# Kernel optimization log

Measured on AMD Instinct MI355X. Metric: run time of the kernel, lower is better.

The kernel has to match this reference:

```python
import jax, jax.numpy as jnp
import numpy as np

EPS = 1e-6  # nn.PairwiseDistance default eps, added as x - y + eps before the norm


def setup_inputs() -> dict:
    key = jax.random.key(0)
    k1, k2 = jax.random.split(key)
    class_prototypes = jax.random.normal(k1, (1024, 1024), dtype=jnp.float32)
    query_features = jax.random.normal(k2, (8192, 1024), dtype=jnp.float32)
    return {"class_prototypes": class_prototypes, "query_features": query_features}


def reference(class_prototypes, query_features):
    # dist[i,k] = || q_i - p_k + EPS ||_2  (PairwiseDistance semantics)
    # expand: ||q||^2 + ||p||^2 - 2 q.p + 2*EPS*(sum q - sum p) + D*EPS^2
    D = query_features.shape[1]
    q_sq = jnp.sum(query_features * query_features, axis=1)        # [Q]
    p_sq = jnp.sum(class_prototypes * class_prototypes, axis=1)    # [K]
    cross = query_features @ class_prototypes.T                    # [Q,K]
    lin = 2.0 * EPS * (jnp.sum(query_features, axis=1)[:, None]
                       - jnp.sum(class_prototypes, axis=1)[None, :])
    sq = q_sq[:, None] + p_sq[None, :] - 2.0 * cross + lin + D * EPS * EPS
    dist = jnp.sqrt(jnp.maximum(sq, 0.0))                          # [Q,K]
    post = jnp.exp(-dist)
    post = post / jnp.sum(post, axis=1, keepdims=True)
    c = jnp.max(post, axis=1)
    h = -jnp.sum(post * jnp.log(post), axis=1)
    return (post, c, h)
```

## Files before the change

### kernel.cpp

```cpp
#include <hip/hip_runtime.h>
#include <hip/hip_bf16.h>

#define EPS 1e-6f

typedef float  f32x4  __attribute__((ext_vector_type(4)));
typedef __bf16 bf16x8 __attribute__((ext_vector_type(8)));

static __device__ __forceinline__ unsigned short f2bf(float f) {
    unsigned int x = __float_as_uint(f);
    unsigned int r = (x + 0x7FFFu + ((x >> 16) & 1u)) >> 16;
    return (unsigned short)r;
}
static __device__ __forceinline__ float bf2f(unsigned short u) {
    return __uint_as_float((unsigned int)u << 16);
}

__global__ __launch_bounds__(256) void prep_kernel(
    const float* __restrict__ protos, const float* __restrict__ querys,
    unsigned short* __restrict__ pb, unsigned short* __restrict__ qb,
    float* __restrict__ p_sq, float* __restrict__ p_sum,
    float* __restrict__ q_sq, float* __restrict__ q_sum)
{
    const int b   = blockIdx.x;
    const int tid = threadIdx.x;
    const float* src; unsigned short* dst; float* rsq; float* rsum;
    if (b < 1024) {
        src = protos + (size_t)b * 1024; dst = pb + (size_t)b * 1024;
        rsq = p_sq + b; rsum = p_sum + b;
    } else {
        const int r = b - 1024;
        src = querys + (size_t)r * 1024; dst = qb + (size_t)r * 1024;
        rsq = q_sq + r; rsum = q_sum + r;
    }

    const float4 v = reinterpret_cast<const float4*>(src)[tid];
    float s  = v.x + v.y + v.z + v.w;
    float ss = v.x * v.x + v.y * v.y + v.z * v.z + v.w * v.w;

    ushort4 o;
    o.x = f2bf(v.x); o.y = f2bf(v.y); o.z = f2bf(v.z); o.w = f2bf(v.w);
    reinterpret_cast<ushort4*>(dst)[tid] = o;

    #pragma unroll
    for (int m = 32; m >= 1; m >>= 1) {
        s  += __shfl_xor(s, m, 64);
        ss += __shfl_xor(ss, m, 64);
    }
    __shared__ float red[8];
    const int wave = tid >> 6;
    if ((tid & 63) == 0) { red[wave] = s; red[4 + wave] = ss; }
    __syncthreads();
    if (tid == 0) {
        *rsum = red[0] + red[1] + red[2] + red[3];
        *rsq  = red[4] + red[5] + red[6] + red[7];
    }
}

__global__ __launch_bounds__(256, 2) void gemm_exp_kernel(
    const unsigned short* __restrict__ qb,
    const unsigned short* __restrict__ pb,
    const float* __restrict__ q_sq, const float* __restrict__ q_sum,
    const float* __restrict__ p_sq, const float* __restrict__ p_sum,
    unsigned short* __restrict__ e_out,
    float* __restrict__ row_s, float* __restrict__ row_t,
    unsigned int* __restrict__ row_m)
{
    __shared__ unsigned short As[128 * 32];
    __shared__ unsigned short Bs[128 * 32];

    const int tid  = threadIdx.x;
    const int lane = tid & 63;
    const int wave = tid >> 6;
    const int wr = wave >> 1, wc = wave & 1;
    const int l15 = lane & 15;
    const int l4  = lane >> 4;
    const int br = blockIdx.x, bc = blockIdx.y;

    f32x4 acc[4][4];
    #pragma unroll
    for (int m = 0; m < 4; ++m)
        #pragma unroll
        for (int n = 0; n < 4; ++n)
            acc[m][n] = (f32x4)0.0f;

    const size_t qbase = (size_t)(br * 128) * 1024;
    const size_t pbase = (size_t)(bc * 128) * 1024;
    const int c0 = tid, c1 = tid + 256;

    for (int kk = 0; kk < 1024; kk += 32) {
        __syncthreads();
        {
            const unsigned short* gq0 = qb + qbase + (size_t)(c0 >> 2) * 1024 + kk + (c0 & 3) * 8;
            const unsigned short* gq1 = qb + qbase + (size_t)(c1 >> 2) * 1024 + kk + (c1 & 3) * 8;
            const unsigned short* gp0 = pb + pbase + (size_t)(c0 >> 2) * 1024 + kk + (c0 & 3) * 8;
            const unsigned short* gp1 = pb + pbase + (size_t)(c1 >> 2) * 1024 + kk + (c1 & 3) * 8;
            __builtin_amdgcn_global_load_lds((const __attribute__((address_space(1))) void*)gq0,
                                             (__attribute__((address_space(3))) void*)(&As[c0 * 8]), 16, 0, 0);
            __builtin_amdgcn_global_load_lds((const __attribute__((address_space(1))) void*)gq1,
                                             (__attribute__((address_space(3))) void*)(&As[c1 * 8]), 16, 0, 0);
            __builtin_amdgcn_global_load_lds((const __attribute__((address_space(1))) void*)gp0,
                                             (__attribute__((address_space(3))) void*)(&Bs[c0 * 8]), 16, 0, 0);
            __builtin_amdgcn_global_load_lds((const __attribute__((address_space(1))) void*)gp1,
                                             (__attribute__((address_space(3))) void*)(&Bs[c1 * 8]), 16, 0, 0);
        }
        __syncthreads();

        bf16x8 a[4], b[4];
        #pragma unroll
        for (int m = 0; m < 4; ++m)
            a[m] = *reinterpret_cast<const bf16x8*>(&As[(wr * 64 + m * 16 + l15) * 32 + l4 * 8]);
        #pragma unroll
        for (int n = 0; n < 4; ++n)
            b[n] = *reinterpret_cast<const bf16x8*>(&Bs[(wc * 64 + n * 16 + l15) * 32 + l4 * 8]);
        #pragma unroll
        for (int m = 0; m < 4; ++m)
            #pragma unroll
            for (int n = 0; n < 4; ++n)
                acc[m][n] = __builtin_amdgcn_mfma_f32_16x16x32_bf16(a[m], b[n], acc[m][n], 0, 0, 0);
    }

    const int row0 = br * 128 + wr * 64;
    const int col0 = bc * 128 + wc * 64;

    float ps[4], pm[4];
    #pragma unroll
    for (int n = 0; n < 4; ++n) {
        const int c = col0 + n * 16 + l15;
        ps[n] = p_sq[c];
        pm[n] = p_sum[c];
    }
    const float dee = 1024.0f * EPS * EPS;

    #pragma unroll
    for (int m = 0; m < 4; ++m) {
        #pragma unroll
        for (int r = 0; r < 4; ++r) {
            const int row = row0 + m * 16 + l4 * 4 + r;
            const float qs = q_sq[row], qm = q_sum[row];
            float se = 0.0f, te = 0.0f, mx = 0.0f;
            #pragma unroll
            for (int n = 0; n < 4; ++n) {
                const float cross = acc[m][n][r];
                const float sq = qs + ps[n] - 2.0f * cross + 2.0f * EPS * (qm - pm[n]) + dee;
                const float dist = sqrtf(fmaxf(sq, 0.0f));
                const float e = __expf(-dist);
                e_out[(size_t)row * 1024 + (col0 + n * 16 + l15)] = f2bf(e);
                se += e;
                te += e * dist;
                mx = fmaxf(mx, e);
            }
            #pragma unroll
            for (int msk = 8; msk >= 1; msk >>= 1) {
                se += __shfl_xor(se, msk, 64);
                te += __shfl_xor(te, msk, 64);
                mx = fmaxf(mx, __shfl_xor(mx, msk, 64));
            }
            if (l15 == 0) {
                atomicAdd(&row_s[row], se);
                atomicAdd(&row_t[row], te);
                atomicMax(&row_m[row], __float_as_uint(mx));
            }
        }
    }
}

__global__ __launch_bounds__(256) void normfin_kernel(
    const unsigned short* __restrict__ e16,
    const float* __restrict__ row_s, const float* __restrict__ row_t,
    const unsigned int* __restrict__ row_m,
    float* __restrict__ post, float* __restrict__ c_out, float* __restrict__ h_out)
{
    const int row = blockIdx.x;
    const int tid = threadIdx.x;
    const float s   = row_s[row];
    const float inv = 1.0f / s;
    if (tid == 0) {
        c_out[row] = __uint_as_float(row_m[row]) * inv;
        h_out[row] = logf(s) + row_t[row] * inv;
    }
    const ushort4 ev = reinterpret_cast<const ushort4*>(e16 + (size_t)row * 1024)[tid];
    float4 o;
    o.x = bf2f(ev.x) * inv;
    o.y = bf2f(ev.y) * inv;
    o.z = bf2f(ev.z) * inv;
    o.w = bf2f(ev.w) * inv;
    reinterpret_cast<float4*>(post + (size_t)row * 1024)[tid] = o;
}

extern "C" void kernel_launch(void* const* d_in, const int* in_sizes, int n_in,
                              void* d_out, int out_size, void* d_ws, size_t ws_size,
                              hipStream_t stream) {
    const float* protos = (const float*)d_in[0];
    const float* querys = (const float*)d_in[1];

    float* out   = (float*)d_out;
    float* post  = out;
    float* c_out = out + (size_t)8192 * 1024;
    float* h_out = c_out + 8192;

    char* ws = (char*)d_ws;
    unsigned short* qb  = (unsigned short*)ws;  ws += (size_t)8192 * 1024 * 2;
    unsigned short* pb  = (unsigned short*)ws;  ws += (size_t)1024 * 1024 * 2;
    unsigned short* e16 = (unsigned short*)ws;  ws += (size_t)8192 * 1024 * 2;
    float* q_sq  = (float*)ws;  ws += 8192 * 4;
    float* q_sum = (float*)ws;  ws += 8192 * 4;
    float* p_sq  = (float*)ws;  ws += 1024 * 4;
    float* p_sum = (float*)ws;  ws += 1024 * 4;
    float* row_s = (float*)ws;  ws += 8192 * 4;
    float* row_t = (float*)ws;  ws += 8192 * 4;
    unsigned int* row_m = (unsigned int*)ws;  ws += 8192 * 4;

    (void)hipMemsetAsync(row_s, 0, 3 * 8192 * sizeof(float), stream);

    prep_kernel<<<9216, 256, 0, stream>>>(protos, querys, pb, qb, p_sq, p_sum, q_sq, q_sum);
    gemm_exp_kernel<<<dim3(64, 8), 256, 0, stream>>>(qb, pb, q_sq, q_sum, p_sq, p_sum,
                                                     e16, row_s, row_t, row_m);
    normfin_kernel<<<8192, 256, 0, stream>>>(e16, row_s, row_t, row_m, post, c_out, h_out);
}
```

Before: 132.4 us.

## Fuse GEMM-exp and normalization into one cooperative kernel with grid sync

Merges the GEMM/exp kernel and the normalization kernel into a single cooperative launch. The exp values stay in accumulator registers across a grid-wide sync and are then scaled by the reciprocal row sum and written directly as fp32 post. This removes the bf16 intermediate round trip through global memory and one kernel launch. In exchange it adds a grid barrier and requires all 512 blocks to be co-resident. It also changes precision slightly, since post is no longer quantized through bf16.

Result: slower. 201.2 us (+52.0%).

```diff
diff --git a/kernel.cpp b/kernel.cpp
--- a/kernel.cpp
+++ b/kernel.cpp
@@ -1,5 +1,8 @@
 #include <hip/hip_runtime.h>
 #include <hip/hip_bf16.h>
+#include <hip/hip_cooperative_groups.h>
+
+namespace cg = cooperative_groups;
 
 #define EPS 1e-6f
 
@@ -10,9 +13,6 @@
     unsigned int x = __float_as_uint(f);
     unsigned int r = (x + 0x7FFFu + ((x >> 16) & 1u)) >> 16;
     return (unsigned short)r;
-}
-static __device__ __forceinline__ float bf2f(unsigned short u) {
-    return __uint_as_float((unsigned int)u << 16);
 }
 
 __global__ __launch_bounds__(256) void prep_kernel(
@@ -56,14 +56,14 @@
     }
 }
 
-__global__ __launch_bounds__(256, 2) void gemm_exp_kernel(
+__global__ __launch_bounds__(256, 2) void coop_kernel(
     const unsigned short* __restrict__ qb,
     const unsigned short* __restrict__ pb,
     const float* __restrict__ q_sq, const float* __restrict__ q_sum,
     const float* __restrict__ p_sq, const float* __restrict__ p_sum,
-    unsigned short* __restrict__ e_out,
     float* __restrict__ row_s, float* __restrict__ row_t,
-    unsigned int* __restrict__ row_m)
+    unsigned int* __restrict__ row_m,
+    float* __restrict__ post, float* __restrict__ c_out, float* __restrict__ h_out)
 {
     __shared__ unsigned short As[128 * 32];
     __shared__ unsigned short Bs[128 * 32];
@@ -144,7 +144,7 @@
                 const float sq = qs + ps[n] - 2.0f * cross + 2.0f * EPS * (qm - pm[n]) + dee;
                 const float dist = sqrtf(fmaxf(sq, 0.0f));
                 const float e = __expf(-dist);
-                e_out[(size_t)row * 1024 + (col0 + n * 16 + l15)] = f2bf(e);
+                acc[m][n][r] = e;
                 se += e;
                 te += e * dist;
                 mx = fmaxf(mx, e);
@@ -162,29 +162,29 @@
             }
         }
     }
-}
-
-__global__ __launch_bounds__(256) void normfin_kernel(
-    const unsigned short* __restrict__ e16,
-    const float* __restrict__ row_s, const float* __restrict__ row_t,
-    const unsigned int* __restrict__ row_m,
-    float* __restrict__ post, float* __restrict__ c_out, float* __restrict__ h_out)
-{
-    const int row = blockIdx.x;
-    const int tid = threadIdx.x;
-    const float s   = row_s[row];
-    const float inv = 1.0f / s;
-    if (tid == 0) {
+
+    cg::this_grid().sync();
+
+    #pragma unroll
+    for (int m = 0; m < 4; ++m) {
+        #pragma unroll
+        for (int r = 0; r < 4; ++r) {
+            const int row = row0 + m * 16 + l4 * 4 + r;
+            const float inv = 1.0f / row_s[row];
+            #pragma unroll
+            for (int n = 0; n < 4; ++n) {
+                post[(size_t)row * 1024 + (col0 + n * 16 + l15)] = acc[m][n][r] * inv;
+            }
+        }
+    }
+
+    if (bc == 0 && tid < 128) {
+        const int row = br * 128 + tid;
+        const float s   = row_s[row];
+        const float inv = 1.0f / s;
         c_out[row] = __uint_as_float(row_m[row]) * inv;
         h_out[row] = logf(s) + row_t[row] * inv;
     }
-    const ushort4 ev = reinterpret_cast<const ushort4*>(e16 + (size_t)row * 1024)[tid];
-    float4 o;
-    o.x = bf2f(ev.x) * inv;
-    o.y = bf2f(ev.y) * inv;
-    o.z = bf2f(ev.z) * inv;
-    o.w = bf2f(ev.w) * inv;
-    reinterpret_cast<float4*>(post + (size_t)row * 1024)[tid] = o;
 }
 
 extern "C" void kernel_launch(void* const* d_in, const int* in_sizes, int n_in,
@@ -199,9 +199,8 @@
     float* h_out = c_out + 8192;
 
     char* ws = (char*)d_ws;
-    unsigned short* qb  = (unsigned short*)ws;  ws += (size_t)8192 * 1024 * 2;
-    unsigned short* pb  = (unsigned short*)ws;  ws += (size_t)1024 * 1024 * 2;
-    unsigned short* e16 = (unsigned short*)ws;  ws += (size_t)8192 * 1024 * 2;
+    unsigned short* qb = (unsigned short*)ws;  ws += (size_t)8192 * 1024 * 2;
+    unsigned short* pb = (unsigned short*)ws;  ws += (size_t)1024 * 1024 * 2;
     float* q_sq  = (float*)ws;  ws += 8192 * 4;
     float* q_sum = (float*)ws;  ws += 8192 * 4;
     float* p_sq  = (float*)ws;  ws += 1024 * 4;
@@ -213,7 +212,10 @@
     (void)hipMemsetAsync(row_s, 0, 3 * 8192 * sizeof(float), stream);
 
     prep_kernel<<<9216, 256, 0, stream>>>(protos, querys, pb, qb, p_sq, p_sum, q_sq, q_sum);
-    gemm_exp_kernel<<<dim3(64, 8), 256, 0, stream>>>(qb, pb, q_sq, q_sum, p_sq, p_sum,
-                                                     e16, row_s, row_t, row_m);
-    normfin_kernel<<<8192, 256, 0, stream>>>(e16, row_s, row_t, row_m, post, c_out, h_out);
-}
+
+    void* args[] = { (void*)&qb, (void*)&pb, (void*)&q_sq, (void*)&q_sum,
+                     (void*)&p_sq, (void*)&p_sum, (void*)&row_s, (void*)&row_t,
+                     (void*)&row_m, (void*)&post, (void*)&c_out, (void*)&h_out };
+    (void)hipLaunchCooperativeKernel((const void*)coop_kernel, dim3(64, 8), dim3(256),
+                                     args, 0, stream);
+}
```

## Shrink GEMM tile to 128x64, swizzle LDS, and remap blocks for L2 locality

Applied to the files above, without the earlier changes.

Halves the prototype tile width so the GEMM launches 1024 blocks instead of 512, and raises the occupancy hint to 4 blocks per CU. It also XOR-swizzles the K-chunk placement in LDS to reduce bank conflicts on fragment reads. Block ids are remapped so that blocks scheduled together share query rows. The smaller tile lowers arithmetic intensity per LDS load, and the tighter launch bound may cause register pressure.

Measured after the change: 136.8 us. +3.3%, slower.

```diff
diff --git a/kernel.cpp b/kernel.cpp
--- a/kernel.cpp
+++ b/kernel.cpp
@@ -56,7 +56,7 @@
     }
 }
 
-__global__ __launch_bounds__(256, 2) void gemm_exp_kernel(
+__global__ __launch_bounds__(256, 4) void gemm_exp_kernel(
     const unsigned short* __restrict__ qb,
     const unsigned short* __restrict__ pb,
     const float* __restrict__ q_sq, const float* __restrict__ q_sum,
@@ -66,7 +66,7 @@
     unsigned int* __restrict__ row_m)
 {
     __shared__ unsigned short As[128 * 32];
-    __shared__ unsigned short Bs[128 * 32];
+    __shared__ unsigned short Bs[64 * 32];
 
     const int tid  = threadIdx.x;
     const int lane = tid & 63;
@@ -74,57 +74,65 @@
     const int wr = wave >> 1, wc = wave & 1;
     const int l15 = lane & 15;
     const int l4  = lane >> 4;
-    const int br = blockIdx.x, bc = blockIdx.y;
-
-    f32x4 acc[4][4];
+
+    const int hwid  = blockIdx.x + blockIdx.y * 64;
+    const int newid = (hwid & 7) * 128 + (hwid >> 3);
+    const int bx = newid >> 4;
+    const int by = newid & 15;
+
+    f32x4 acc[4][2];
     #pragma unroll
     for (int m = 0; m < 4; ++m)
         #pragma unroll
-        for (int n = 0; n < 4; ++n)
+        for (int n = 0; n < 2; ++n)
             acc[m][n] = (f32x4)0.0f;
 
-    const size_t qbase = (size_t)(br * 128) * 1024;
-    const size_t pbase = (size_t)(bc * 128) * 1024;
-    const int c0 = tid, c1 = tid + 256;
+    const size_t qbase = (size_t)(bx * 128) * 1024;
+    const size_t pbase = (size_t)(by * 64) * 1024;
 
     for (int kk = 0; kk < 1024; kk += 32) {
         __syncthreads();
         {
-            const unsigned short* gq0 = qb + qbase + (size_t)(c0 >> 2) * 1024 + kk + (c0 & 3) * 8;
-            const unsigned short* gq1 = qb + qbase + (size_t)(c1 >> 2) * 1024 + kk + (c1 & 3) * 8;
-            const unsigned short* gp0 = pb + pbase + (size_t)(c0 >> 2) * 1024 + kk + (c0 & 3) * 8;
-            const unsigned short* gp1 = pb + pbase + (size_t)(c1 >> 2) * 1024 + kk + (c1 & 3) * 8;
-            __builtin_amdgcn_global_load_lds((const __attribute__((address_space(1))) void*)gq0,
-                                             (__attribute__((address_space(3))) void*)(&As[c0 * 8]), 16, 0, 0);
-            __builtin_amdgcn_global_load_lds((const __attribute__((address_space(1))) void*)gq1,
-                                             (__attribute__((address_space(3))) void*)(&As[c1 * 8]), 16, 0, 0);
-            __builtin_amdgcn_global_load_lds((const __attribute__((address_space(1))) void*)gp0,
-                                             (__attribute__((address_space(3))) void*)(&Bs[c0 * 8]), 16, 0, 0);
-            __builtin_amdgcn_global_load_lds((const __attribute__((address_space(1))) void*)gp1,
-                                             (__attribute__((address_space(3))) void*)(&Bs[c1 * 8]), 16, 0, 0);
+            const int la0 = tid,      la1 = tid + 256, lb = tid;
+            const int kpa0 = (la0 & 3) ^ ((la0 >> 3) & 3);
+            const int kpa1 = (la1 & 3) ^ ((la1 >> 3) & 3);
+            const int kpb  = (lb  & 3) ^ ((lb  >> 3) & 3);
+            const unsigned short* ga0 = qb + qbase + (size_t)(la0 >> 2) * 1024 + kk + kpa0 * 8;
+            const unsigned short* ga1 = qb + qbase + (size_t)(la1 >> 2) * 1024 + kk + kpa1 * 8;
+            const unsigned short* gb  = pb + pbase + (size_t)(lb  >> 2) * 1024 + kk + kpb  * 8;
+            __builtin_amdgcn_global_load_lds((const __attribute__((address_space(1))) void*)ga0,
+                                             (__attribute__((address_space(3))) void*)(&As[la0 * 8]), 16, 0, 0);
+            __builtin_amdgcn_global_load_lds((const __attribute__((address_space(1))) void*)ga1,
+                                             (__attribute__((address_space(3))) void*)(&As[la1 * 8]), 16, 0, 0);
+            __builtin_amdgcn_global_load_lds((const __attribute__((address_space(1))) void*)gb,
+                                             (__attribute__((address_space(3))) void*)(&Bs[lb * 8]), 16, 0, 0);
         }
         __syncthreads();
 
-        bf16x8 a[4], b[4];
-        #pragma unroll
-        for (int m = 0; m < 4; ++m)
-            a[m] = *reinterpret_cast<const bf16x8*>(&As[(wr * 64 + m * 16 + l15) * 32 + l4 * 8]);
-        #pragma unroll
-        for (int n = 0; n < 4; ++n)
-            b[n] = *reinterpret_cast<const bf16x8*>(&Bs[(wc * 64 + n * 16 + l15) * 32 + l4 * 8]);
+        bf16x8 a[4], b[2];
+        #pragma unroll
+        for (int m = 0; m < 4; ++m) {
+            const int rowA = wr * 64 + m * 16 + l15;
+            a[m] = *reinterpret_cast<const bf16x8*>(&As[rowA * 32 + (l4 ^ ((rowA >> 1) & 3)) * 8]);
+        }
+        #pragma unroll
+        for (int n = 0; n < 2; ++n) {
+            const int rowB = wc * 32 + n * 16 + l15;
+            b[n] = *reinterpret_cast<const bf16x8*>(&Bs[rowB * 32 + (l4 ^ ((rowB >> 1) & 3)) * 8]);
+        }
         #pragma unroll
         for (int m = 0; m < 4; ++m)
             #pragma unroll
-            for (int n = 0; n < 4; ++n)
+            for (int n = 0; n < 2; ++n)
                 acc[m][n] = __builtin_amdgcn_mfma_f32_16x16x32_bf16(a[m], b[n], acc[m][n], 0, 0, 0);
     }
 
-    const int row0 = br * 128 + wr * 64;
-    const int col0 = bc * 128 + wc * 64;
-
-    float ps[4], pm[4];
-    #pragma unroll
-    for (int n = 0; n < 4; ++n) {
+    const int row0 = bx * 128 + wr * 64;
+    const int col0 = by * 64 + wc * 32;
+
+    float ps[2], pm[2];
+    #pragma unroll
+    for (int n = 0; n < 2; ++n) {
         const int c = col0 + n * 16 + l15;
         ps[n] = p_sq[c];
         pm[n] = p_sum[c];
@@ -139,7 +147,7 @@
             const float qs = q_sq[row], qm = q_sum[row];
             float se = 0.0f, te = 0.0f, mx = 0.0f;
             #pragma unroll
-            for (int n = 0; n < 4; ++n) {
+            for (int n = 0; n < 2; ++n) {
                 const float cross = acc[m][n][r];
                 const float sq = qs + ps[n] - 2.0f * cross + 2.0f * EPS * (qm - pm[n]) + dee;
                 const float dist = sqrtf(fmaxf(sq, 0.0f));
@@ -213,7 +221,7 @@
     (void)hipMemsetAsync(row_s, 0, 3 * 8192 * sizeof(float), stream);
 
     prep_kernel<<<9216, 256, 0, stream>>>(protos, querys, pb, qb, p_sq, p_sum, q_sq, q_sum);
-    gemm_exp_kernel<<<dim3(64, 8), 256, 0, stream>>>(qb, pb, q_sq, q_sum, p_sq, p_sum,
-                                                     e16, row_s, row_t, row_m);
+    gemm_exp_kernel<<<dim3(64, 16), 256, 0, stream>>>(qb, pb, q_sq, q_sum, p_sq, p_sum,
+                                                      e16, row_s, row_t, row_m);
     normfin_kernel<<<8192, 256, 0, stream>>>(e16, row_s, row_t, row_m, post, c_out, h_out);
 }
```

## Double GEMM K-tile, XOR-swizzle LDS layout, remap block order for locality

Applied to the files above, without the earlier changes.

Raises the K step per iteration from 32 to 64, which halves the number of barrier-synchronized load phases. The LDS tiles get an XOR swizzle on the 16-byte column group so the fragment reads avoid bank conflicts. Block IDs are remapped so that consecutively scheduled blocks are spread across XCDs, with neighbouring tiles grouped for L2 reuse. The cost is twice the shared memory per block, which may limit occupancy, and there is still no double buffering.

Measured after the change: 129.7 us. 1.02x faster.

```diff
diff --git a/kernel.cpp b/kernel.cpp
--- a/kernel.cpp
+++ b/kernel.cpp
@@ -65,8 +65,8 @@
     float* __restrict__ row_s, float* __restrict__ row_t,
     unsigned int* __restrict__ row_m)
 {
-    __shared__ unsigned short As[128 * 32];
-    __shared__ unsigned short Bs[128 * 32];
+    __shared__ unsigned short As[128 * 64];
+    __shared__ unsigned short Bs[128 * 64];
 
     const int tid  = threadIdx.x;
     const int lane = tid & 63;
@@ -74,7 +74,11 @@
     const int wr = wave >> 1, wc = wave & 1;
     const int l15 = lane & 15;
     const int l4  = lane >> 4;
-    const int br = blockIdx.x, bc = blockIdx.y;
+
+    const int hwid  = blockIdx.x + blockIdx.y * 64;
+    const int newid = (hwid & 7) * 64 + (hwid >> 3);
+    const int bx = newid >> 3;
+    const int by = newid & 7;
 
     f32x4 acc[4][4];
     #pragma unroll
@@ -83,44 +87,50 @@
         for (int n = 0; n < 4; ++n)
             acc[m][n] = (f32x4)0.0f;
 
-    const size_t qbase = (size_t)(br * 128) * 1024;
-    const size_t pbase = (size_t)(bc * 128) * 1024;
-    const int c0 = tid, c1 = tid + 256;
-
-    for (int kk = 0; kk < 1024; kk += 32) {
+    const size_t qbase = (size_t)(bx * 128) * 1024;
+    const size_t pbase = (size_t)(by * 128) * 1024;
+
+    for (int kk = 0; kk < 1024; kk += 64) {
         __syncthreads();
-        {
-            const unsigned short* gq0 = qb + qbase + (size_t)(c0 >> 2) * 1024 + kk + (c0 & 3) * 8;
-            const unsigned short* gq1 = qb + qbase + (size_t)(c1 >> 2) * 1024 + kk + (c1 & 3) * 8;
-            const unsigned short* gp0 = pb + pbase + (size_t)(c0 >> 2) * 1024 + kk + (c0 & 3) * 8;
-            const unsigned short* gp1 = pb + pbase + (size_t)(c1 >> 2) * 1024 + kk + (c1 & 3) * 8;
-            __builtin_amdgcn_global_load_lds((const __attribute__((address_space(1))) void*)gq0,
-                                             (__attribute__((address_space(3))) void*)(&As[c0 * 8]), 16, 0, 0);
-            __builtin_amdgcn_global_load_lds((const __attribute__((address_space(1))) void*)gq1,
-                                             (__attribute__((address_space(3))) void*)(&As[c1 * 8]), 16, 0, 0);
-            __builtin_amdgcn_global_load_lds((const __attribute__((address_space(1))) void*)gp0,
-                                             (__attribute__((address_space(3))) void*)(&Bs[c0 * 8]), 16, 0, 0);
-            __builtin_amdgcn_global_load_lds((const __attribute__((address_space(1))) void*)gp1,
-                                             (__attribute__((address_space(3))) void*)(&Bs[c1 * 8]), 16, 0, 0);
+        #pragma unroll
+        for (int i = 0; i < 4; ++i) {
+            const int lin = i * 256 + tid;
+            const int row = lin >> 3;
+            const int cg  = (lin & 7) ^ (row & 7);
+            const unsigned short* ga = qb + qbase + (size_t)row * 1024 + kk + cg * 8;
+            const unsigned short* gb = pb + pbase + (size_t)row * 1024 + kk + cg * 8;
+            __builtin_amdgcn_global_load_lds((const __attribute__((address_space(1))) void*)ga,
+                                             (__attribute__((address_space(3))) void*)(&As[lin * 8]), 16, 0, 0);
+            __builtin_amdgcn_global_load_lds((const __attribute__((address_space(1))) void*)gb,
+                                             (__attribute__((address_space(3))) void*)(&Bs[lin * 8]), 16, 0, 0);
         }
         __syncthreads();
 
-        bf16x8 a[4], b[4];
-        #pragma unroll
-        for (int m = 0; m < 4; ++m)
-            a[m] = *reinterpret_cast<const bf16x8*>(&As[(wr * 64 + m * 16 + l15) * 32 + l4 * 8]);
-        #pragma unroll
-        for (int n = 0; n < 4; ++n)
-            b[n] = *reinterpret_cast<const bf16x8*>(&Bs[(wc * 64 + n * 16 + l15) * 32 + l4 * 8]);
-        #pragma unroll
-        for (int m = 0; m < 4; ++m)
-            #pragma unroll
-            for (int n = 0; n < 4; ++n)
-                acc[m][n] = __builtin_amdgcn_mfma_f32_16x16x32_bf16(a[m], b[n], acc[m][n], 0, 0, 0);
-    }
-
-    const int row0 = br * 128 + wr * 64;
-    const int col0 = bc * 128 + wc * 64;
+        #pragma unroll
+        for (int s = 0; s < 2; ++s) {
+            bf16x8 a[4], b[4];
+            #pragma unroll
+            for (int m = 0; m < 4; ++m) {
+                const int rowA = wr * 64 + m * 16 + l15;
+                const int ca = (s * 4 + l4) ^ (rowA & 7);
+                a[m] = *reinterpret_cast<const bf16x8*>(&As[rowA * 64 + ca * 8]);
+            }
+            #pragma unroll
+            for (int n = 0; n < 4; ++n) {
+                const int rowB = wc * 64 + n * 16 + l15;
+                const int cb = (s * 4 + l4) ^ (rowB & 7);
+                b[n] = *reinterpret_cast<const bf16x8*>(&Bs[rowB * 64 + cb * 8]);
+            }
+            #pragma unroll
+            for (int m = 0; m < 4; ++m)
+                #pragma unroll
+                for (int n = 0; n < 4; ++n)
+                    acc[m][n] = __builtin_amdgcn_mfma_f32_16x16x32_bf16(a[m], b[n], acc[m][n], 0, 0, 0);
+        }
+    }
+
+    const int row0 = bx * 128 + wr * 64;
+    const int col0 = by * 128 + wc * 64;
 
     float ps[4], pm[4];
     #pragma unroll
```
